# Kernel optimization log

Hardware: AMD Instinct MI355X
Metric: run time of the kernel (lower is better)

Reference implementation:

```python
import jax, jax.numpy as jnp
import numpy as np

N = 50000      # nodes
E = 800000     # directed edges (avg degree 16)
IN, HID, OUT = 128, 128, 64


def setup_inputs() -> dict:
    key = jax.random.key(0)
    k1, k2, k3, k4 = jax.random.split(key, 4)
    x = jax.random.normal(k1, (N, IN), dtype=jnp.float32)
    edge_index = jax.random.randint(k2, (2, E), 0, N, dtype=jnp.int64)
    W1 = jax.random.normal(k3, (IN, HID), dtype=jnp.float32) * (1.0 / np.sqrt(IN))
    b1 = jnp.zeros((HID,), dtype=jnp.float32)
    W2 = jax.random.normal(k4, (HID, OUT), dtype=jnp.float32) * (1.0 / np.sqrt(HID))
    b2 = jnp.zeros((OUT,), dtype=jnp.float32)
    return {"x": x, "edge_index": edge_index, "W1": W1, "b1": b1, "W2": W2, "b2": b2}


def _gcn_conv(x, src, dst, norm, W, b, n):
    # linear transform first (PyG GCNConv), then normalized scatter-add aggregation
    h = x @ W                                  # [N, d_out]
    msg = h[src] * norm[:, None]               # [E', d_out] gathered edge messages
    return jax.ops.segment_sum(msg, dst, num_segments=n) + b


def reference(x, edge_index, W1, b1, W2, b2):
    n = x.shape[0]
    loops = jnp.arange(n, dtype=edge_index.dtype)
    src = jnp.concatenate([edge_index[0], loops])  # source (row)
    dst = jnp.concatenate([edge_index[1], loops])  # target (col)
    # symmetric normalization on A + I: deg over destination nodes
    deg = jax.ops.segment_sum(jnp.ones_like(src, dtype=x.dtype), dst, num_segments=n)
    dinv = jnp.where(deg > 0, jax.lax.rsqrt(deg), 0.0)
    norm = dinv[src] * dinv[dst]               # [E']
    h = jax.nn.relu(_gcn_conv(x, src, dst, norm, W1, b1, n))
    out = _gcn_conv(h, src, dst, norm, W2, b2, n)
    return jax.nn.log_softmax(out, axis=1)
```

## Files before the change

kernel.cpp:

```cpp
#include <hip/hip_runtime.h>


constexpr int K1 = 128;
constexpr int SCAN_B = 256;

typedef short short8 __attribute__((ext_vector_type(8)));
typedef float f32x4 __attribute__((ext_vector_type(4)));

__device__ inline unsigned short f2b(float f) {
    unsigned u = __float_as_uint(f);
    u += 0x7fffu + ((u >> 16) & 1u);
    return (unsigned short)(u >> 16);
}

__global__ void k_zero(int* __restrict__ deg, int n) {
    int i = blockIdx.x * blockDim.x + threadIdx.x;
    if (i < n) deg[i] = 0;
}

__global__ void k_count_w(const int* __restrict__ dst, int e, int* __restrict__ deg,
                          unsigned short* __restrict__ rank,
                          const float* __restrict__ W1, const float* __restrict__ W2,
                          unsigned short* __restrict__ w1bt,
                          unsigned short* __restrict__ w2bt, int nwcvt) {
    int b = blockIdx.x;
    if (b < nwcvt) {
        int i = b * blockDim.x + threadIdx.x;
        if (i < 128 * 128) {
            int c = i >> 7, k = i & 127;
            w1bt[i] = f2b(W1[k * 128 + c]);
        }
        if (i < 64 * 128) {
            int c = i >> 7, k = i & 127;
            w2bt[i] = f2b(W2[k * 64 + c]);
        }
    } else {
        int i = (b - nwcvt) * blockDim.x + threadIdx.x;
        if (i < e) {
            int p = atomicAdd(&deg[dst[i]], 1);
            rank[i] = (unsigned short)p;
        }
    }
}

__global__ __launch_bounds__(SCAN_B) void k_scan_part(const int* __restrict__ deg,
                                                      int* __restrict__ blocksum, int n) {
    __shared__ int red[SCAN_B];
    int i = blockIdx.x * SCAN_B + threadIdx.x;
    int v = (i < n) ? deg[i] : 0;
    red[threadIdx.x] = v;
    __syncthreads();
    for (int o = SCAN_B / 2; o; o >>= 1) {
        if (threadIdx.x < o) red[threadIdx.x] += red[threadIdx.x + o];
        __syncthreads();
    }
    if (threadIdx.x == 0) blocksum[blockIdx.x] = red[0];
}

__global__ __launch_bounds__(1024) void k_scan_top(int* __restrict__ blocksum, int nb) {
    __shared__ int sh[1024];
    int t = threadIdx.x;
    int v = (t < nb) ? blocksum[t] : 0;
    sh[t] = v;
    __syncthreads();
    for (int o = 1; o < 1024; o <<= 1) {
        int u = (t >= o) ? sh[t - o] : 0;
        __syncthreads();
        sh[t] += u;
        __syncthreads();
    }
    if (t < nb) blocksum[t] = sh[t] - v;
}

__global__ __launch_bounds__(SCAN_B) void k_scan_final(const int* __restrict__ deg,
                                                       const int* __restrict__ blocksum,
                                                       int* __restrict__ off,
                                                       float* __restrict__ dinv, int n) {
    __shared__ int sh[SCAN_B];
    int t = threadIdx.x;
    int i = blockIdx.x * SCAN_B + t;
    int v = (i < n) ? deg[i] : 0;
    sh[t] = v;
    __syncthreads();
    for (int o = 1; o < SCAN_B; o <<= 1) {
        int u = (t >= o) ? sh[t - o] : 0;
        __syncthreads();
        sh[t] += u;
        __syncthreads();
    }
    if (i < n) {
        off[i] = blocksum[blockIdx.x] + sh[t] - v;
        dinv[i] = rsqrtf((float)(v + 1));
    }
}

__device__ __forceinline__ void gemm128_body(int bid, const float* __restrict__ A,
                                             const unsigned short* __restrict__ Wbt,
                                             const float* __restrict__ dinv,
                                             unsigned short* __restrict__ Cb, int n) {
    constexpr int NT = 8;
    const int tid = threadIdx.x;
    const int wave = tid >> 6, lane = tid & 63;
    const int rowbase = bid * 128 + wave * 32;
    const int lrow = lane & 15;
    const int kgrp = lane >> 4;

    short8 a[2][4];
#pragma unroll
    for (int s = 0; s < 2; ++s)
#pragma unroll
        for (int kt = 0; kt < 4; ++kt) {
            int R = rowbase + 16 * s + lrow;
            int Rc = (R < n) ? R : (n - 1);
            const float* p = A + (size_t)Rc * 128 + kt * 32 + kgrp * 8;
            float4 u0 = *reinterpret_cast<const float4*>(p);
            float4 u1 = *reinterpret_cast<const float4*>(p + 4);
            short8 af;
            af[0] = (short)f2b(u0.x); af[1] = (short)f2b(u0.y);
            af[2] = (short)f2b(u0.z); af[3] = (short)f2b(u0.w);
            af[4] = (short)f2b(u1.x); af[5] = (short)f2b(u1.y);
            af[6] = (short)f2b(u1.z); af[7] = (short)f2b(u1.w);
            a[s][kt] = af;
        }

    f32x4 acc[2][NT];
#pragma unroll
    for (int s = 0; s < 2; ++s)
#pragma unroll
        for (int nt = 0; nt < NT; ++nt) acc[s][nt] = f32x4{0.f, 0.f, 0.f, 0.f};

#pragma unroll
    for (int nt = 0; nt < NT; ++nt) {
        short8 b[4];
#pragma unroll
        for (int kt = 0; kt < 4; ++kt)
            b[kt] = *reinterpret_cast<const short8*>(
                Wbt + (size_t)(nt * 16 + lrow) * 128 + kt * 32 + kgrp * 8);
#pragma unroll
        for (int s = 0; s < 2; ++s)
#pragma unroll
            for (int kt = 0; kt < 4; ++kt)
                acc[s][nt] = __builtin_amdgcn_mfma_f32_16x16x32_bf16(a[s][kt], b[kt],
                                                                     acc[s][nt], 0, 0, 0);
    }

#pragma unroll
    for (int s = 0; s < 2; ++s)
#pragma unroll
        for (int r = 0; r < 4; ++r) {
            int R = rowbase + 16 * s + kgrp * 4 + r;
            if (R < n) {
                float sc = dinv[R];
#pragma unroll
                for (int nt = 0; nt < NT; ++nt)
                    Cb[(size_t)R * 128 + nt * 16 + lrow] = f2b(sc * acc[s][nt][r]);
            }
        }
}

__global__ __launch_bounds__(256) void k_gemm64(
    const unsigned short* __restrict__ Ab, const unsigned short* __restrict__ Wbt,
    const float* __restrict__ dinv, unsigned short* __restrict__ Cb, int n) {
    constexpr int NT = 4;
    const int tid = threadIdx.x;
    const int wave = tid >> 6, lane = tid & 63;
    const int rowbase = blockIdx.x * 128 + wave * 32;
    const int lrow = lane & 15;
    const int kgrp = lane >> 4;

    short8 a[2][4];
#pragma unroll
    for (int s = 0; s < 2; ++s)
#pragma unroll
        for (int kt = 0; kt < 4; ++kt) {
            int R = rowbase + 16 * s + lrow;
            int Rc = (R < n) ? R : (n - 1);
            a[s][kt] = *reinterpret_cast<const short8*>(
                Ab + (size_t)Rc * 128 + kt * 32 + kgrp * 8);
        }

    f32x4 acc[2][NT];
#pragma unroll
    for (int s = 0; s < 2; ++s)
#pragma unroll
        for (int nt = 0; nt < NT; ++nt) acc[s][nt] = f32x4{0.f, 0.f, 0.f, 0.f};

#pragma unroll
    for (int nt = 0; nt < NT; ++nt) {
        short8 b[4];
#pragma unroll
        for (int kt = 0; kt < 4; ++kt)
            b[kt] = *reinterpret_cast<const short8*>(
                Wbt + (size_t)(nt * 16 + lrow) * 128 + kt * 32 + kgrp * 8);
#pragma unroll
        for (int s = 0; s < 2; ++s)
#pragma unroll
            for (int kt = 0; kt < 4; ++kt)
                acc[s][nt] = __builtin_amdgcn_mfma_f32_16x16x32_bf16(a[s][kt], b[kt],
                                                                     acc[s][nt], 0, 0, 0);
    }

#pragma unroll
    for (int s = 0; s < 2; ++s)
#pragma unroll
        for (int r = 0; r < 4; ++r) {
            int R = rowbase + 16 * s + kgrp * 4 + r;
            if (R < n) {
                float sc = dinv[R];
#pragma unroll
                for (int nt = 0; nt < NT; ++nt)
                    Cb[(size_t)R * 64 + nt * 16 + lrow] = f2b(sc * acc[s][nt][r]);
            }
        }
}

__global__ __launch_bounds__(256) void k_gemm_fill(
    const float* __restrict__ A, const unsigned short* __restrict__ Wbt,
    const float* __restrict__ dinv, unsigned short* __restrict__ Cb, int n,
    const int* __restrict__ src, const int* __restrict__ dst,
    const unsigned short* __restrict__ rank, const int* __restrict__ off,
    unsigned short* __restrict__ csr, int e, int ngemm) {
    int b = blockIdx.x;
    if (b < ngemm) {
        gemm128_body(b, A, Wbt, dinv, Cb, n);
    } else {
        int i = (b - ngemm) * blockDim.x + threadIdx.x;
        if (i < e) csr[off[dst[i]] + rank[i]] = (unsigned short)src[i];
    }
}

__global__ __launch_bounds__(256) void k_gather128(
    const int* __restrict__ off, const int* __restrict__ deg,
    const unsigned short* __restrict__ csr, const unsigned short* __restrict__ xb,
    const float* __restrict__ dinv, const float* __restrict__ b,
    unsigned short* __restrict__ agg, int n) {
    int wid = (blockIdx.x * blockDim.x + threadIdx.x) >> 6;
    int lane = threadIdx.x & 63;
    if (wid >= n) return;
    const int q = lane >> 4;
    const int c0 = (lane & 15) * 8;

    float a[8];
#pragma unroll
    for (int k = 0; k < 8; ++k) a[k] = 0.f;

    const int s0 = off[wid];
    const int cnt = deg[wid];

    int t = q;
    for (; t + 4 < cnt; t += 8) {
        int e0 = csr[s0 + t];
        int e1 = csr[s0 + t + 4];
        uint4 v0 = *reinterpret_cast<const uint4*>(xb + (size_t)e0 * 128 + c0);
        uint4 v1 = *reinterpret_cast<const uint4*>(xb + (size_t)e1 * 128 + c0);
#pragma unroll
        for (int j = 0; j < 4; ++j) {
            unsigned w0 = (&v0.x)[j];
            unsigned w1 = (&v1.x)[j];
            a[2 * j]     += __uint_as_float(w0 << 16);
            a[2 * j + 1] += __uint_as_float(w0 & 0xffff0000u);
            a[2 * j]     += __uint_as_float(w1 << 16);
            a[2 * j + 1] += __uint_as_float(w1 & 0xffff0000u);
        }
    }
    for (; t < cnt; t += 4) {
        int e0 = csr[s0 + t];
        uint4 v0 = *reinterpret_cast<const uint4*>(xb + (size_t)e0 * 128 + c0);
#pragma unroll
        for (int j = 0; j < 4; ++j) {
            unsigned w0 = (&v0.x)[j];
            a[2 * j]     += __uint_as_float(w0 << 16);
            a[2 * j + 1] += __uint_as_float(w0 & 0xffff0000u);
        }
    }

#pragma unroll
    for (int k = 0; k < 8; ++k) {
        a[k] += __shfl_xor(a[k], 16);
        a[k] += __shfl_xor(a[k], 32);
    }

    if (q == 0) {
        float di = dinv[wid];
        uint4 sv = *reinterpret_cast<const uint4*>(xb + (size_t)wid * 128 + c0);
        float4 bv0 = *reinterpret_cast<const float4*>(b + c0);
        float4 bv1 = *reinterpret_cast<const float4*>(b + c0 + 4);
        float o[8];
#pragma unroll
        for (int j = 0; j < 4; ++j) {
            unsigned w = (&sv.x)[j];
            o[2 * j]     = a[2 * j]     + __uint_as_float(w << 16);
            o[2 * j + 1] = a[2 * j + 1] + __uint_as_float(w & 0xffff0000u);
        }
        const float* bb0 = (const float*)&bv0;
        const float* bb1 = (const float*)&bv1;
        short8 st;
#pragma unroll
        for (int k = 0; k < 8; ++k) {
            float bk = (k < 4) ? bb0[k] : bb1[k - 4];
            st[k] = (short)f2b(fmaxf(fmaf(di, o[k], bk), 0.f));
        }
        *reinterpret_cast<short8*>(agg + (size_t)wid * 128 + c0) = st;
    }
}

__global__ __launch_bounds__(256) void k_gather64_lsm(
    const int* __restrict__ off, const int* __restrict__ deg,
    const unsigned short* __restrict__ csr, const unsigned short* __restrict__ hb,
    const float* __restrict__ dinv, const float* __restrict__ b,
    float* __restrict__ out, int n) {
    int wid = (blockIdx.x * blockDim.x + threadIdx.x) >> 6;
    int lane = threadIdx.x & 63;
    if (wid >= n) return;
    const int oct = lane >> 3;
    const int c0 = (lane & 7) * 8;

    float a[8];
#pragma unroll
    for (int k = 0; k < 8; ++k) a[k] = 0.f;

    const int s0 = off[wid];
    const int cnt = deg[wid];

    int t = oct;
    for (; t + 8 < cnt; t += 16) {
        int e0 = csr[s0 + t];
        int e1 = csr[s0 + t + 8];
        uint4 v0 = *reinterpret_cast<const uint4*>(hb + (size_t)e0 * 64 + c0);
        uint4 v1 = *reinterpret_cast<const uint4*>(hb + (size_t)e1 * 64 + c0);
#pragma unroll
        for (int j = 0; j < 4; ++j) {
            unsigned w0 = (&v0.x)[j];
            unsigned w1 = (&v1.x)[j];
            a[2 * j]     += __uint_as_float(w0 << 16);
            a[2 * j + 1] += __uint_as_float(w0 & 0xffff0000u);
            a[2 * j]     += __uint_as_float(w1 << 16);
            a[2 * j + 1] += __uint_as_float(w1 & 0xffff0000u);
        }
    }
    for (; t < cnt; t += 8) {
        int e0 = csr[s0 + t];
        uint4 v0 = *reinterpret_cast<const uint4*>(hb + (size_t)e0 * 64 + c0);
#pragma unroll
        for (int j = 0; j < 4; ++j) {
            unsigned w0 = (&v0.x)[j];
            a[2 * j]     += __uint_as_float(w0 << 16);
            a[2 * j + 1] += __uint_as_float(w0 & 0xffff0000u);
        }
    }

#pragma unroll
    for (int k = 0; k < 8; ++k) {
        a[k] += __shfl_xor(a[k], 8);
        a[k] += __shfl_xor(a[k], 16);
        a[k] += __shfl_xor(a[k], 32);
    }

    float di = dinv[wid];
    uint4 sv = *reinterpret_cast<const uint4*>(hb + (size_t)wid * 64 + c0);
    float4 bv0 = *reinterpret_cast<const float4*>(b + c0);
    float4 bv1 = *reinterpret_cast<const float4*>(b + c0 + 4);
    float v[8];
#pragma unroll
    for (int j = 0; j < 4; ++j) {
        unsigned w = (&sv.x)[j];
        v[2 * j]     = a[2 * j]     + __uint_as_float(w << 16);
        v[2 * j + 1] = a[2 * j + 1] + __uint_as_float(w & 0xffff0000u);
    }
    v[0] = fmaf(di, v[0], bv0.x);
    v[1] = fmaf(di, v[1], bv0.y);
    v[2] = fmaf(di, v[2], bv0.z);
    v[3] = fmaf(di, v[3], bv0.w);
    v[4] = fmaf(di, v[4], bv1.x);
    v[5] = fmaf(di, v[5], bv1.y);
    v[6] = fmaf(di, v[6], bv1.z);
    v[7] = fmaf(di, v[7], bv1.w);

    float m = v[0];
#pragma unroll
    for (int k = 1; k < 8; ++k) m = fmaxf(m, v[k]);
    m = fmaxf(m, __shfl_xor(m, 1));
    m = fmaxf(m, __shfl_xor(m, 2));
    m = fmaxf(m, __shfl_xor(m, 4));

    float s = 0.f;
#pragma unroll
    for (int k = 0; k < 8; ++k) s += expf(v[k] - m);
    s += __shfl_xor(s, 1);
    s += __shfl_xor(s, 2);
    s += __shfl_xor(s, 4);
    float ls = m + logf(s);

    if (oct == 0) {
        float4 r0, r1;
        r0.x = v[0] - ls; r0.y = v[1] - ls; r0.z = v[2] - ls; r0.w = v[3] - ls;
        r1.x = v[4] - ls; r1.y = v[5] - ls; r1.z = v[6] - ls; r1.w = v[7] - ls;
        *reinterpret_cast<float4*>(out + (size_t)wid * 64 + c0) = r0;
        *reinterpret_cast<float4*>(out + (size_t)wid * 64 + c0 + 4) = r1;
    }
}

extern "C" void kernel_launch(void* const* d_in, const int* in_sizes, int n_in,
                              void* d_out, int out_size, void* d_ws, size_t ws_size,
                              hipStream_t stream) {
    const float* x  = (const float*)d_in[0];
    const int*   ei = (const int*)d_in[1];
    const float* W1 = (const float*)d_in[2];
    const float* b1 = (const float*)d_in[3];
    const float* W2 = (const float*)d_in[4];
    const float* b2 = (const float*)d_in[5];

    const int n = in_sizes[0] / K1;
    const int e = in_sizes[1] / 2;
    const int* src = ei;
    const int* dst = ei + e;
    float* out = (float*)d_out;

    const int nb_scan = (n + SCAN_B - 1) / SCAN_B;
    const int ngemm = (n + 127) / 128;
    const int ncount = (e + 255) / 256;
    const int nwcvt = (128 * 128 + 255) / 256;

    unsigned short* agg1     = (unsigned short*)d_ws;
    unsigned short* xb16     = agg1 + (size_t)n * 128;
    unsigned short* hb16     = xb16 + (size_t)n * 128;
    int*            deg      = (int*)(hb16 + (size_t)n * 64);
    float*          dinv     = (float*)(deg + n);
    int*            off      = (int*)(dinv + n);
    int*            blocksum = off + n;
    unsigned short* w1bt     = (unsigned short*)(((uintptr_t)(blocksum + nb_scan) + 15) &
                                                 ~(uintptr_t)15);
    unsigned short* w2bt     = w1bt + 128 * 128;
    unsigned short* rank     = w2bt + 64 * 128;
    unsigned short* csr      = rank + e;

    const int B = 256;

    k_zero<<<(n + B - 1) / B, B, 0, stream>>>(deg, n);
    k_count_w<<<nwcvt + ncount, B, 0, stream>>>(dst, e, deg, rank, W1, W2,
                                                w1bt, w2bt, nwcvt);
    k_scan_part<<<nb_scan, SCAN_B, 0, stream>>>(deg, blocksum, n);
    k_scan_top<<<1, 1024, 0, stream>>>(blocksum, nb_scan);
    k_scan_final<<<nb_scan, SCAN_B, 0, stream>>>(deg, blocksum, off, dinv, n);

    k_gemm_fill<<<ngemm + ncount, B, 0, stream>>>(x, w1bt, dinv, xb16, n,
                                                  src, dst, rank, off, csr, e, ngemm);

    k_gather128<<<(n + 3) / 4, B, 0, stream>>>(off, deg, csr, xb16, dinv, b1, agg1, n);

    k_gemm64<<<ngemm, B, 0, stream>>>(agg1, w2bt, dinv, hb16, n);
    k_gather64_lsm<<<(n + 3) / 4, B, 0, stream>>>(off, deg, csr, hb16, dinv, b2, out, n);
}
```

Before: 145.0 us.

## Move dinv scaling into gather so first GEMM overlaps degree counting

The first GEMM no longer multiplies by the source dinv. The gather applies dinv per neighbour with an FMA instead. This lets the GEMM run in the same launch as the atomic degree count, and the weight conversion merges into the zero-init kernel. The top-level scan is folded into scan_final, where each block redundantly scans the block sums (this assumes nb_scan <= 256). The cost is an extra dinv load per edge in the layer-1 gather, and the CSR fill now runs as its own launch.

```diff
diff --git a/kernel.cpp b/kernel.cpp
--- a/kernel.cpp
+++ b/kernel.cpp
@@ -13,90 +13,23 @@
     return (unsigned short)(u >> 16);
 }
 
-__global__ void k_zero(int* __restrict__ deg, int n) {
+__global__ void k_init(int* __restrict__ deg, const float* __restrict__ W1,
+                       const float* __restrict__ W2, unsigned short* __restrict__ w1bt,
+                       unsigned short* __restrict__ w2bt, int n) {
     int i = blockIdx.x * blockDim.x + threadIdx.x;
     if (i < n) deg[i] = 0;
-}
-
-__global__ void k_count_w(const int* __restrict__ dst, int e, int* __restrict__ deg,
-                          unsigned short* __restrict__ rank,
-                          const float* __restrict__ W1, const float* __restrict__ W2,
-                          unsigned short* __restrict__ w1bt,
-                          unsigned short* __restrict__ w2bt, int nwcvt) {
-    int b = blockIdx.x;
-    if (b < nwcvt) {
-        int i = b * blockDim.x + threadIdx.x;
-        if (i < 128 * 128) {
-            int c = i >> 7, k = i & 127;
-            w1bt[i] = f2b(W1[k * 128 + c]);
-        }
-        if (i < 64 * 128) {
-            int c = i >> 7, k = i & 127;
-            w2bt[i] = f2b(W2[k * 64 + c]);
-        }
-    } else {
-        int i = (b - nwcvt) * blockDim.x + threadIdx.x;
-        if (i < e) {
-            int p = atomicAdd(&deg[dst[i]], 1);
-            rank[i] = (unsigned short)p;
-        }
-    }
-}
-
-__global__ __launch_bounds__(SCAN_B) void k_scan_part(const int* __restrict__ deg,
-                                                      int* __restrict__ blocksum, int n) {
-    __shared__ int red[SCAN_B];
-    int i = blockIdx.x * SCAN_B + threadIdx.x;
-    int v = (i < n) ? deg[i] : 0;
-    red[threadIdx.x] = v;
-    __syncthreads();
-    for (int o = SCAN_B / 2; o; o >>= 1) {
-        if (threadIdx.x < o) red[threadIdx.x] += red[threadIdx.x + o];
-        __syncthreads();
-    }
-    if (threadIdx.x == 0) blocksum[blockIdx.x] = red[0];
-}
-
-__global__ __launch_bounds__(1024) void k_scan_top(int* __restrict__ blocksum, int nb) {
-    __shared__ int sh[1024];
-    int t = threadIdx.x;
-    int v = (t < nb) ? blocksum[t] : 0;
-    sh[t] = v;
-    __syncthreads();
-    for (int o = 1; o < 1024; o <<= 1) {
-        int u = (t >= o) ? sh[t - o] : 0;
-        __syncthreads();
-        sh[t] += u;
-        __syncthreads();
-    }
-    if (t < nb) blocksum[t] = sh[t] - v;
-}
-
-__global__ __launch_bounds__(SCAN_B) void k_scan_final(const int* __restrict__ deg,
-                                                       const int* __restrict__ blocksum,
-                                                       int* __restrict__ off,
-                                                       float* __restrict__ dinv, int n) {
-    __shared__ int sh[SCAN_B];
-    int t = threadIdx.x;
-    int i = blockIdx.x * SCAN_B + t;
-    int v = (i < n) ? deg[i] : 0;
-    sh[t] = v;
-    __syncthreads();
-    for (int o = 1; o < SCAN_B; o <<= 1) {
-        int u = (t >= o) ? sh[t - o] : 0;
-        __syncthreads();
-        sh[t] += u;
-        __syncthreads();
-    }
-    if (i < n) {
-        off[i] = blocksum[blockIdx.x] + sh[t] - v;
-        dinv[i] = rsqrtf((float)(v + 1));
+    if (i < 128 * 128) {
+        int c = i >> 7, k = i & 127;
+        w1bt[i] = f2b(W1[k * 128 + c]);
+    }
+    if (i < 64 * 128) {
+        int c = i >> 7, k = i & 127;
+        w2bt[i] = f2b(W2[k * 64 + c]);
     }
 }
 
 __device__ __forceinline__ void gemm128_body(int bid, const float* __restrict__ A,
                                              const unsigned short* __restrict__ Wbt,
-                                             const float* __restrict__ dinv,
                                              unsigned short* __restrict__ Cb, int n) {
     constexpr int NT = 8;
     const int tid = threadIdx.x;
@@ -150,12 +83,84 @@
         for (int r = 0; r < 4; ++r) {
             int R = rowbase + 16 * s + kgrp * 4 + r;
             if (R < n) {
-                float sc = dinv[R];
 #pragma unroll
                 for (int nt = 0; nt < NT; ++nt)
-                    Cb[(size_t)R * 128 + nt * 16 + lrow] = f2b(sc * acc[s][nt][r]);
+                    Cb[(size_t)R * 128 + nt * 16 + lrow] = f2b(acc[s][nt][r]);
             }
         }
+}
+
+__global__ __launch_bounds__(256) void k_count_gemm(
+    const int* __restrict__ dst, int e, int* __restrict__ deg,
+    unsigned short* __restrict__ rank, const float* __restrict__ A,
+    const unsigned short* __restrict__ Wbt, unsigned short* __restrict__ Cb,
+    int n, int ncount) {
+    int b = blockIdx.x;
+    if (b < ncount) {
+        int i = b * blockDim.x + threadIdx.x;
+        if (i < e) {
+            int p = atomicAdd(&deg[dst[i]], 1);
+            rank[i] = (unsigned short)p;
+        }
+    } else {
+        gemm128_body(b - ncount, A, Wbt, Cb, n);
+    }
+}
+
+__global__ __launch_bounds__(SCAN_B) void k_scan_part(const int* __restrict__ deg,
+                                                      int* __restrict__ blocksum, int n) {
+    __shared__ int red[SCAN_B];
+    int i = blockIdx.x * SCAN_B + threadIdx.x;
+    int v = (i < n) ? deg[i] : 0;
+    red[threadIdx.x] = v;
+    __syncthreads();
+    for (int o = SCAN_B / 2; o; o >>= 1) {
+        if (threadIdx.x < o) red[threadIdx.x] += red[threadIdx.x + o];
+        __syncthreads();
+    }
+    if (threadIdx.x == 0) blocksum[blockIdx.x] = red[0];
+}
+
+__global__ __launch_bounds__(SCAN_B) void k_scan_final(const int* __restrict__ deg,
+                                                       const int* __restrict__ blocksum,
+                                                       int nb, int* __restrict__ off,
+                                                       float* __restrict__ dinv, int n) {
+    __shared__ int sh[SCAN_B];
+    __shared__ int bs[SCAN_B];
+    int t = threadIdx.x;
+
+    bs[t] = (t < nb) ? blocksum[t] : 0;
+    __syncthreads();
+    for (int o = 1; o < SCAN_B; o <<= 1) {
+        int u = (t >= o) ? bs[t - o] : 0;
+        __syncthreads();
+        bs[t] += u;
+        __syncthreads();
+    }
+    const int base = (blockIdx.x > 0) ? bs[blockIdx.x - 1] : 0;
+
+    int i = blockIdx.x * SCAN_B + t;
+    int v = (i < n) ? deg[i] : 0;
+    sh[t] = v;
+    __syncthreads();
+    for (int o = 1; o < SCAN_B; o <<= 1) {
+        int u = (t >= o) ? sh[t - o] : 0;
+        __syncthreads();
+        sh[t] += u;
+        __syncthreads();
+    }
+    if (i < n) {
+        off[i] = base + sh[t] - v;
+        dinv[i] = rsqrtf((float)(v + 1));
+    }
+}
+
+__global__ void k_fill(const int* __restrict__ src, const int* __restrict__ dst,
+                       const unsigned short* __restrict__ rank,
+                       const int* __restrict__ off,
+                       unsigned short* __restrict__ csr, int e) {
+    int i = blockIdx.x * blockDim.x + threadIdx.x;
+    if (i < e) csr[off[dst[i]] + rank[i]] = (unsigned short)src[i];
 }
 
 __global__ __launch_bounds__(256) void k_gemm64(
@@ -212,21 +217,6 @@
                     Cb[(size_t)R * 64 + nt * 16 + lrow] = f2b(sc * acc[s][nt][r]);
             }
         }
-}
-
-__global__ __launch_bounds__(256) void k_gemm_fill(
-    const float* __restrict__ A, const unsigned short* __restrict__ Wbt,
-    const float* __restrict__ dinv, unsigned short* __restrict__ Cb, int n,
-    const int* __restrict__ src, const int* __restrict__ dst,
-    const unsigned short* __restrict__ rank, const int* __restrict__ off,
-    unsigned short* __restrict__ csr, int e, int ngemm) {
-    int b = blockIdx.x;
-    if (b < ngemm) {
-        gemm128_body(b, A, Wbt, dinv, Cb, n);
-    } else {
-        int i = (b - ngemm) * blockDim.x + threadIdx.x;
-        if (i < e) csr[off[dst[i]] + rank[i]] = (unsigned short)src[i];
-    }
 }
 
 __global__ __launch_bounds__(256) void k_gather128(
@@ -251,26 +241,29 @@
     for (; t + 4 < cnt; t += 8) {
         int e0 = csr[s0 + t];
         int e1 = csr[s0 + t + 4];
+        float d0 = dinv[e0];
+        float d1 = dinv[e1];
         uint4 v0 = *reinterpret_cast<const uint4*>(xb + (size_t)e0 * 128 + c0);
         uint4 v1 = *reinterpret_cast<const uint4*>(xb + (size_t)e1 * 128 + c0);
 #pragma unroll
         for (int j = 0; j < 4; ++j) {
             unsigned w0 = (&v0.x)[j];
             unsigned w1 = (&v1.x)[j];
-            a[2 * j]     += __uint_as_float(w0 << 16);
-            a[2 * j + 1] += __uint_as_float(w0 & 0xffff0000u);
-            a[2 * j]     += __uint_as_float(w1 << 16);
-            a[2 * j + 1] += __uint_as_float(w1 & 0xffff0000u);
+            a[2 * j]     = fmaf(d0, __uint_as_float(w0 << 16), a[2 * j]);
+            a[2 * j + 1] = fmaf(d0, __uint_as_float(w0 & 0xffff0000u), a[2 * j + 1]);
+            a[2 * j]     = fmaf(d1, __uint_as_float(w1 << 16), a[2 * j]);
+            a[2 * j + 1] = fmaf(d1, __uint_as_float(w1 & 0xffff0000u), a[2 * j + 1]);
         }
     }
     for (; t < cnt; t += 4) {
         int e0 = csr[s0 + t];
+        float d0 = dinv[e0];
         uint4 v0 = *reinterpret_cast<const uint4*>(xb + (size_t)e0 * 128 + c0);
 #pragma unroll
         for (int j = 0; j < 4; ++j) {
             unsigned w0 = (&v0.x)[j];
-            a[2 * j]     += __uint_as_float(w0 << 16);
-            a[2 * j + 1] += __uint_as_float(w0 & 0xffff0000u);
+            a[2 * j]     = fmaf(d0, __uint_as_float(w0 << 16), a[2 * j]);
+            a[2 * j + 1] = fmaf(d0, __uint_as_float(w0 & 0xffff0000u), a[2 * j + 1]);
         }
     }
 
@@ -289,8 +282,8 @@
 #pragma unroll
         for (int j = 0; j < 4; ++j) {
             unsigned w = (&sv.x)[j];
-            o[2 * j]     = a[2 * j]     + __uint_as_float(w << 16);
-            o[2 * j + 1] = a[2 * j + 1] + __uint_as_float(w & 0xffff0000u);
+            o[2 * j]     = fmaf(di, __uint_as_float(w << 16), a[2 * j]);
+            o[2 * j + 1] = fmaf(di, __uint_as_float(w & 0xffff0000u), a[2 * j + 1]);
         }
         const float* bb0 = (const float*)&bv0;
         const float* bb1 = (const float*)&bv1;
@@ -419,7 +412,6 @@
     const int nb_scan = (n + SCAN_B - 1) / SCAN_B;
     const int ngemm = (n + 127) / 128;
     const int ncount = (e + 255) / 256;
-    const int nwcvt = (128 * 128 + 255) / 256;
 
     unsigned short* agg1     = (unsigned short*)d_ws;
     unsigned short* xb16     = agg1 + (size_t)n * 128;
@@ -436,18 +428,13 @@
 
     const int B = 256;
 
-    k_zero<<<(n + B - 1) / B, B, 0, stream>>>(deg, n);
-    k_count_w<<<nwcvt + ncount, B, 0, stream>>>(dst, e, deg, rank, W1, W2,
-                                                w1bt, w2bt, nwcvt);
+    k_init<<<(n + B - 1) / B, B, 0, stream>>>(deg, W1, W2, w1bt, w2bt, n);
+    k_count_gemm<<<ncount + ngemm, B, 0, stream>>>(dst, e, deg, rank, x, w1bt,
+                                                   xb16, n, ncount);
     k_scan_part<<<nb_scan, SCAN_B, 0, stream>>>(deg, blocksum, n);
-    k_scan_top<<<1, 1024, 0, stream>>>(blocksum, nb_scan);
-    k_scan_final<<<nb_scan, SCAN_B, 0, stream>>>(deg, blocksum, off, dinv, n);
-
-    k_gemm_fill<<<ngemm + ncount, B, 0, stream>>>(x, w1bt, dinv, xb16, n,
-                                                  src, dst, rank, off, csr, e, ngemm);
-
+    k_scan_final<<<nb_scan, SCAN_B, 0, stream>>>(deg, blocksum, nb_scan, off, dinv, n);
+    k_fill<<<ncount, B, 0, stream>>>(src, dst, rank, off, csr, e);
     k_gather128<<<(n + 3) / 4, B, 0, stream>>>(off, deg, csr, xb16, dinv, b1, agg1, n);
-
     k_gemm64<<<ngemm, B, 0, stream>>>(agg1, w2bt, dinv, hb16, n);
     k_gather64_lsm<<<(n + 3) / 4, B, 0, stream>>>(off, deg, csr, hb16, dinv, b2, out, n);
 }
```

Result: slower. 153.9 us (+6.1%).
